# Kernel optimization log

Measured on AMD Instinct MI355X. Metric: run time of the kernel, lower is better.

The kernel has to match this reference:

```python
import jax, jax.numpy as jnp
import numpy as np

BLOCK = 128
FP8_MAX = 448.0  # max representable value of float8_e4m3fn
F8 = jnp.float8_e4m3fn


def setup_inputs() -> dict:
    key = jax.random.key(0)
    k1, k2, k3 = jax.random.split(key, 3)
    M, K, N = 4096, 7168, 16384
    x = jax.random.normal(k1, (M, K), jnp.float32)
    w = jax.random.normal(k2, (N, K), jnp.float32)  # raw weight; cast to fp8 in reference to simulate stored fp8
    w_scale = jax.random.uniform(k3, (N // BLOCK, K // BLOCK), jnp.float32, 0.5, 1.5)
    return {"x": x, "w": w, "w_scale": w_scale, "block_size": BLOCK}


def act_quant(x, b):
    M, K = x.shape
    xb = x.reshape(M, K // b, b)
    s = jnp.max(jnp.abs(xb), axis=-1) / FP8_MAX  # [M, K//b]
    xq = (xb / s[..., None]).astype(F8).astype(jnp.float32).reshape(M, K)
    return xq, s


def reference(x, w, w_scale, block_size):
    b = block_size
    # simulate fp8-stored weight (element_size == 1 branch)
    w8 = w.astype(F8).astype(jnp.float32)  # [N, K]
    # fp8_gemm: y[m,n] = sum_k xq[m,k]*w8[n,k]*xs[m,kb]*ws[nb,kb]
    # scales factor per-element, so dequantize both operands then one dense GEMM
    xq, xs = act_quant(x, b)
    x_dq = xq * jnp.repeat(xs, b, axis=1)                         # [M, K]
    w_dq = w8 * jnp.repeat(jnp.repeat(w_scale, b, axis=0), b, axis=1)  # [N, K]
    return x_dq @ w_dq.T  # [M, N], no bias (bias=False)
```

## Files before the change

kernel.cpp:

```cpp
#include <hip/hip_runtime.h>
#include <hip/hip_bf16.h>
#include <hip/hip_fp8.h>

typedef __attribute__((ext_vector_type(4))) float f32x4;
typedef __attribute__((ext_vector_type(2))) long long ll2;

#define AS1 __attribute__((address_space(1)))
#define AS3 __attribute__((address_space(3)))

static constexpr int Mdim = 4096;
static constexpr int Kdim = 7168;
static constexpr int Ndim = 16384;
static constexpr int KB   = Kdim / 128;
static constexpr float FP8_MAX = 448.0f;

#define BARRIER() do { asm volatile("" ::: "memory"); \
                       __builtin_amdgcn_s_barrier();  \
                       asm volatile("" ::: "memory"); } while (0)

#define MFMA_FP8 __builtin_amdgcn_mfma_f32_16x16x32_fp8_fp8

__global__ __launch_bounds__(256) void quant_x_kernel(
    const float* __restrict__ x, unsigned char* __restrict__ xq,
    float* __restrict__ xst)
{
    constexpr int NBLK = Mdim * KB;
    const int lane = threadIdx.x & 63;
    const int wid  = (blockIdx.x * 256 + threadIdx.x) >> 6;
    const int nw   = (gridDim.x * 256) >> 6;

    for (int b = wid; b < NBLK; b += nw) {
        size_t base = (size_t)b * 128 + lane * 2;
        float2 v = *reinterpret_cast<const float2*>(x + base);
        float amax = fmaxf(fabsf(v.x), fabsf(v.y));
#pragma unroll
        for (int off = 32; off > 0; off >>= 1)
            amax = fmaxf(amax, __shfl_xor(amax, off));
        float s = amax * (1.0f / FP8_MAX);
        unsigned char q0 = 0, q1 = 0;
        if (s > 0.0f) {
            q0 = __hip_fp8_e4m3(v.x / s).__x;
            q1 = __hip_fp8_e4m3(v.y / s).__x;
        }
        *reinterpret_cast<unsigned short*>(xq + base) =
            (unsigned short)(q0 | ((unsigned short)q1 << 8));
        if (lane == 0) {
            int row = b / KB, kb = b - row * KB;
            xst[(size_t)kb * Mdim + row] = s;
        }
    }
}

__global__ __launch_bounds__(256) void quant_w_kernel(
    const float* __restrict__ w, unsigned char* __restrict__ w8)
{
    constexpr size_t NCHUNK = (size_t)Ndim * Kdim / 8;

    size_t idx    = (size_t)blockIdx.x * 256 + threadIdx.x;
    size_t stride = (size_t)gridDim.x * 256;

    for (size_t c = idx; c < NCHUNK; c += stride) {
        const float* src = w + c * 8;
        float4 v0 = *reinterpret_cast<const float4*>(src);
        float4 v1 = *reinterpret_cast<const float4*>(src + 4);
        unsigned int lo = (unsigned int)__hip_fp8_e4m3(v0.x).__x
                        | ((unsigned int)__hip_fp8_e4m3(v0.y).__x << 8)
                        | ((unsigned int)__hip_fp8_e4m3(v0.z).__x << 16)
                        | ((unsigned int)__hip_fp8_e4m3(v0.w).__x << 24);
        unsigned int hi = (unsigned int)__hip_fp8_e4m3(v1.x).__x
                        | ((unsigned int)__hip_fp8_e4m3(v1.y).__x << 8)
                        | ((unsigned int)__hip_fp8_e4m3(v1.z).__x << 16)
                        | ((unsigned int)__hip_fp8_e4m3(v1.w).__x << 24);
        uint2 p; p.x = lo; p.y = hi;
        *reinterpret_cast<uint2*>(w8 + c * 8) = p;
    }
}

constexpr int BM = 256, BN = 256, BK = 64;
constexpr int NT  = Kdim / BK;
constexpr int NBN = Ndim / BN;
constexpr int NWG = (Mdim / BM) * NBN;
constexpr int K1  = Kdim;
constexpr int XS_OFF = 65536;
constexpr int WS_OFF = XS_OFF + 56 * 1024;
constexpr int LDS_TOT = WS_OFF + 448;

__global__ __launch_bounds__(512, 2) void gemm256_fp8_kernel(
    const unsigned char* __restrict__ Ag,
    const unsigned char* __restrict__ Bg,
    const float* __restrict__ xsT,
    const float* __restrict__ Wsc,
    float* __restrict__ C)
{
    extern __shared__ char smem[];

    const int tid  = threadIdx.x;
    const int w    = tid >> 6;
    const int lane = tid & 63;
    const int wr   = w >> 2;
    const int wc   = w & 3;
    const int lr   = lane & 15;
    const int lk   = lane >> 4;

    int bid = (int)blockIdx.x;
    int swz = (bid & 7) * (NWG >> 3) + (bid >> 3);
    const int bm = (swz / NBN) * BM;
    const int bn = (swz % NBN) * BN;

    const int colF = (lk ^ ((lr >> 1) & 3)) << 4;
    const int bRow = (wc & 1) * 64;

    const char* xsL0 = smem + XS_OFF + (wr * 128 + lk * 4) * 4;
    const char* wsL  = smem + WS_OFF + (wc >> 1) * (KB * 4);

    const int rowS = tid >> 2;
    const int colS = (((tid & 3) ^ ((rowS >> 1) & 3))) * 16;
    const size_t offG = (size_t)rowS * K1 + colS;
    const int ldsW = tid * 16;

    const char* Ab = (const char*)Ag + (size_t)bm * K1;
    const char* Bb = (const char*)Bg + (size_t)bn * K1;

    auto stage = [&](int j) {
        if (j >= 4 * NT) return;
        const int T    = j >> 2;
        const int r    = j & 3;
        const int isA  = r >> 1;
        const int half = r & 1;
        const int regByte = (T & 1) * 32768 + (isA ? 0 : 16384) + half * 8192;
        const char* g = (isA ? Ab : Bb) + (size_t)half * (128 * (size_t)K1)
                        + (size_t)T * 64 + offG;
        __builtin_amdgcn_global_load_lds((const AS1 void*)g,
                                         (AS3 void*)(smem + regByte + ldsW),
                                         16, 0, 0);
    };

#pragma unroll
    for (int i = 0; i < 7; ++i) {
        const int kb = w * 7 + i;
        const float* g = xsT + (size_t)kb * Mdim + bm + lane * 4;
        __builtin_amdgcn_global_load_lds((const AS1 void*)g,
            (AS3 void*)(smem + XS_OFF + kb * 1024), 16, 0, 0);
    }
    if (w == 0 && lane < 28) {
        const float* g = Wsc + (size_t)(bn >> 7) * KB + lane * 4;
        __builtin_amdgcn_global_load_lds((const AS1 void*)g,
            (AS3 void*)(smem + WS_OFF), 16, 0, 0);
    }
    for (int j = 0; j < 6; ++j) stage(j);
    asm volatile("s_waitcnt vmcnt(2)" ::: "memory");
    BARRIER();

    f32x4 acc[8][4] = {};

    for (int t = 0; t < NT; ++t) {
        const int buf = t & 1;
        const int kb  = t >> 1;
        const char* aB = smem + buf * 32768 + wr * 8192;
        const char* bB = smem + buf * 32768 + 16384 + (wc >> 1) * 8192;
        ll2 a0[4], a1[4], b0[2], b1[2];
        f32x4 sv[4];

        const float wsv  = *(const float*)(wsL + kb * 4);
        const char* xsLk = xsL0 + (kb << 10);

        stage(4 * t + 6);
#pragma unroll
        for (int m = 0; m < 4; ++m)
            a0[m] = *(const ll2*)(aB + (m * 16 + lr) * 64 + colF);
#pragma unroll
        for (int n = 0; n < 2; ++n)
            b0[n] = *(const ll2*)(bB + (bRow + n * 16 + lr) * 64 + colF);
#pragma unroll
        for (int m = 0; m < 4; ++m)
            sv[m] = *reinterpret_cast<const f32x4*>(xsLk + m * 64) * wsv;
        __builtin_amdgcn_s_setprio(1);
#pragma unroll
        for (int m = 0; m < 4; ++m)
#pragma unroll
            for (int n = 0; n < 2; ++n) {
                f32x4 pacc = {0.f, 0.f, 0.f, 0.f};
                pacc = MFMA_FP8(a0[m][0], b0[n][0], pacc, 0, 0, 0);
                pacc = MFMA_FP8(a0[m][1], b0[n][1], pacc, 0, 0, 0);
                acc[m][n] += sv[m] * pacc;
            }
        __builtin_amdgcn_s_setprio(0);

        stage(4 * t + 7);
#pragma unroll
        for (int n = 0; n < 2; ++n)
            b1[n] = *(const ll2*)(bB + (bRow + (n + 2) * 16 + lr) * 64 + colF);
        __builtin_amdgcn_s_setprio(1);
#pragma unroll
        for (int m = 0; m < 4; ++m)
#pragma unroll
            for (int n = 0; n < 2; ++n) {
                f32x4 pacc = {0.f, 0.f, 0.f, 0.f};
                pacc = MFMA_FP8(a0[m][0], b1[n][0], pacc, 0, 0, 0);
                pacc = MFMA_FP8(a0[m][1], b1[n][1], pacc, 0, 0, 0);
                acc[m][n + 2] += sv[m] * pacc;
            }
        __builtin_amdgcn_s_setprio(0);
        BARRIER();

        stage(4 * t + 8);
#pragma unroll
        for (int m = 0; m < 4; ++m)
            a1[m] = *(const ll2*)(aB + ((m + 4) * 16 + lr) * 64 + colF);
#pragma unroll
        for (int m = 0; m < 4; ++m)
            sv[m] = *reinterpret_cast<const f32x4*>(xsLk + 256 + m * 64) * wsv;
        __builtin_amdgcn_s_setprio(1);
#pragma unroll
        for (int m = 0; m < 4; ++m)
#pragma unroll
            for (int n = 0; n < 2; ++n) {
                f32x4 pacc = {0.f, 0.f, 0.f, 0.f};
                pacc = MFMA_FP8(a1[m][0], b0[n][0], pacc, 0, 0, 0);
                pacc = MFMA_FP8(a1[m][1], b0[n][1], pacc, 0, 0, 0);
                acc[m + 4][n] += sv[m] * pacc;
            }
        __builtin_amdgcn_s_setprio(0);

        stage(4 * t + 9);
        __builtin_amdgcn_s_setprio(1);
#pragma unroll
        for (int m = 0; m < 4; ++m)
#pragma unroll
            for (int n = 0; n < 2; ++n) {
                f32x4 pacc = {0.f, 0.f, 0.f, 0.f};
                pacc = MFMA_FP8(a1[m][0], b1[n][0], pacc, 0, 0, 0);
                pacc = MFMA_FP8(a1[m][1], b1[n][1], pacc, 0, 0, 0);
                acc[m + 4][n + 2] += sv[m] * pacc;
            }
        __builtin_amdgcn_s_setprio(0);
        if (t < NT - 2) { asm volatile("s_waitcnt vmcnt(2)" ::: "memory"); }
        else            { asm volatile("s_waitcnt vmcnt(0)" ::: "memory"); }
        BARRIER();
    }

#pragma unroll
    for (int m = 0; m < 8; ++m) {
#pragma unroll
        for (int n = 0; n < 4; ++n) {
            const int row0 = bm + wr * 128 + m * 16 + lk * 4;
            const int col  = bn + wc * 64 + n * 16 + lr;
#pragma unroll
            for (int j = 0; j < 4; ++j)
                C[(size_t)(row0 + j) * Ndim + col] = acc[m][n][j];
        }
    }
}

extern "C" void kernel_launch(void* const* d_in, const int* in_sizes, int n_in,
                              void* d_out, int out_size, void* d_ws, size_t ws_size,
                              hipStream_t stream) {
    const float* x  = (const float*)d_in[0];
    const float* w  = (const float*)d_in[1];
    const float* ws = (const float*)d_in[2];

    unsigned char* xq  = (unsigned char*)d_ws;
    unsigned char* w8  = xq + (size_t)Mdim * Kdim;
    float*         xst = (float*)(w8 + (size_t)Ndim * Kdim);

    quant_x_kernel<<<2048, 256, 0, stream>>>(x, xq, xst);
    quant_w_kernel<<<4096, 256, 0, stream>>>(w, w8);

    hipFuncSetAttribute((const void*)gemm256_fp8_kernel,
                        hipFuncAttributeMaxDynamicSharedMemorySize, LDS_TOT);
    gemm256_fp8_kernel<<<NWG, 512, LDS_TOT, stream>>>(xq, w8, xst, ws,
                                                      (float*)d_out);
}
```

Baseline: 1.044 ms.

## Shrink GEMM tile to 128x256 and restructure LDS staging pipeline

```diff
diff --git a/kernel.cpp b/kernel.cpp
--- a/kernel.cpp
+++ b/kernel.cpp
@@ -76,16 +76,17 @@
     }
 }
 
-constexpr int BM = 256, BN = 256, BK = 64;
+constexpr int BM = 128, BN = 256, BK = 64;
 constexpr int NT  = Kdim / BK;
 constexpr int NBN = Ndim / BN;
 constexpr int NWG = (Mdim / BM) * NBN;
 constexpr int K1  = Kdim;
-constexpr int XS_OFF = 65536;
-constexpr int WS_OFF = XS_OFF + 56 * 1024;
+constexpr int BUFSZ  = 24576;
+constexpr int XS_OFF = 49152;
+constexpr int WS_OFF = XS_OFF + 56 * 512;
 constexpr int LDS_TOT = WS_OFF + 448;
 
-__global__ __launch_bounds__(512, 2) void gemm256_fp8_kernel(
+__global__ __launch_bounds__(512, 2) void gemm128_fp8_kernel(
     const unsigned char* __restrict__ Ag,
     const unsigned char* __restrict__ Bg,
     const float* __restrict__ xsT,
@@ -108,27 +109,24 @@
     const int bn = (swz % NBN) * BN;
 
     const int colF = (lk ^ ((lr >> 1) & 3)) << 4;
+    const int aRow = wr * 64;
     const int bRow = (wc & 1) * 64;
 
-    const char* xsL0 = smem + XS_OFF + (wr * 128 + lk * 4) * 4;
+    const char* xsL0 = smem + XS_OFF + (wr * 64 + lk * 4) * 4;
     const char* wsL  = smem + WS_OFF + (wc >> 1) * (KB * 4);
 
     const int rowS = tid >> 2;
     const int colS = (((tid & 3) ^ ((rowS >> 1) & 3))) * 16;
     const size_t offG = (size_t)rowS * K1 + colS;
-    const int ldsW = tid * 16;
+    const int ldsW = w * 1024;
 
     const char* Ab = (const char*)Ag + (size_t)bm * K1;
     const char* Bb = (const char*)Bg + (size_t)bn * K1;
 
-    auto stage = [&](int j) {
-        if (j >= 4 * NT) return;
-        const int T    = j >> 2;
-        const int r    = j & 3;
-        const int isA  = r >> 1;
-        const int half = r & 1;
-        const int regByte = (T & 1) * 32768 + (isA ? 0 : 16384) + half * 8192;
-        const char* g = (isA ? Ab : Bb) + (size_t)half * (128 * (size_t)K1)
+    auto stage = [&](int T, int r) {
+        if (T >= NT) return;
+        const int regByte = (T & 1) * BUFSZ + r * 8192;
+        const char* g = (r ? Bb + (size_t)(r - 1) * (128 * (size_t)K1) : Ab)
                         + (size_t)T * 64 + offG;
         __builtin_amdgcn_global_load_lds((const AS1 void*)g,
                                          (AS3 void*)(smem + regByte + ldsW),
@@ -136,42 +134,50 @@
     };
 
 #pragma unroll
-    for (int i = 0; i < 7; ++i) {
-        const int kb = w * 7 + i;
-        const float* g = xsT + (size_t)kb * Mdim + bm + lane * 4;
-        __builtin_amdgcn_global_load_lds((const AS1 void*)g,
-            (AS3 void*)(smem + XS_OFF + kb * 1024), 16, 0, 0);
+    for (int i = 0; i < 4; ++i) {
+        const int c = i * 8 + w;
+        if (c < 28) {
+            const int kb  = 2 * c + (lane >> 5);
+            const int row = (lane & 31) * 4;
+            const float* g = xsT + (size_t)kb * Mdim + bm + row;
+            __builtin_amdgcn_global_load_lds((const AS1 void*)g,
+                (AS3 void*)(smem + XS_OFF + c * 1024), 16, 0, 0);
+        }
     }
     if (w == 0 && lane < 28) {
         const float* g = Wsc + (size_t)(bn >> 7) * KB + lane * 4;
         __builtin_amdgcn_global_load_lds((const AS1 void*)g,
             (AS3 void*)(smem + WS_OFF), 16, 0, 0);
     }
-    for (int j = 0; j < 6; ++j) stage(j);
+    stage(0, 0); stage(0, 1); stage(0, 2);
+    stage(1, 1); stage(1, 2);
     asm volatile("s_waitcnt vmcnt(2)" ::: "memory");
     BARRIER();
 
-    f32x4 acc[8][4] = {};
+    f32x4 acc[4][4] = {};
 
     for (int t = 0; t < NT; ++t) {
         const int buf = t & 1;
         const int kb  = t >> 1;
-        const char* aB = smem + buf * 32768 + wr * 8192;
-        const char* bB = smem + buf * 32768 + 16384 + (wc >> 1) * 8192;
-        ll2 a0[4], a1[4], b0[2], b1[2];
+        const char* aB = smem + buf * BUFSZ;
+        const char* bB = smem + buf * BUFSZ + 8192 + (wc >> 1) * 8192;
+        ll2 a[4], b0[2], b1[2];
         f32x4 sv[4];
 
         const float wsv  = *(const float*)(wsL + kb * 4);
-        const char* xsLk = xsL0 + (kb << 10);
-
-        stage(4 * t + 6);
-#pragma unroll
-        for (int m = 0; m < 4; ++m)
-            a0[m] = *(const ll2*)(aB + (m * 16 + lr) * 64 + colF);
+        const char* xsLk = xsL0 + kb * 512;
+
+        stage(t + 1, 0);
+#pragma unroll
+        for (int m = 0; m < 4; ++m)
+            a[m] = *(const ll2*)(aB + (aRow + m * 16 + lr) * 64 + colF);
 #pragma unroll
         for (int n = 0; n < 2; ++n)
             b0[n] = *(const ll2*)(bB + (bRow + n * 16 + lr) * 64 + colF);
 #pragma unroll
+        for (int n = 0; n < 2; ++n)
+            b1[n] = *(const ll2*)(bB + (bRow + (n + 2) * 16 + lr) * 64 + colF);
+#pragma unroll
         for (int m = 0; m < 4; ++m)
             sv[m] = *reinterpret_cast<const f32x4*>(xsLk + m * 64) * wsv;
         __builtin_amdgcn_s_setprio(1);
@@ -180,58 +186,25 @@
 #pragma unroll
             for (int n = 0; n < 2; ++n) {
                 f32x4 pacc = {0.f, 0.f, 0.f, 0.f};
-                pacc = MFMA_FP8(a0[m][0], b0[n][0], pacc, 0, 0, 0);
-                pacc = MFMA_FP8(a0[m][1], b0[n][1], pacc, 0, 0, 0);
+                pacc = MFMA_FP8(a[m][0], b0[n][0], pacc, 0, 0, 0);
+                pacc = MFMA_FP8(a[m][1], b0[n][1], pacc, 0, 0, 0);
                 acc[m][n] += sv[m] * pacc;
             }
         __builtin_amdgcn_s_setprio(0);
-
-        stage(4 * t + 7);
-#pragma unroll
-        for (int n = 0; n < 2; ++n)
-            b1[n] = *(const ll2*)(bB + (bRow + (n + 2) * 16 + lr) * 64 + colF);
+        asm volatile("s_waitcnt lgkmcnt(0)" ::: "memory");
+        BARRIER();
+
+        stage(t + 2, 1);
+        stage(t + 2, 2);
         __builtin_amdgcn_s_setprio(1);
 #pragma unroll
         for (int m = 0; m < 4; ++m)
 #pragma unroll
             for (int n = 0; n < 2; ++n) {
                 f32x4 pacc = {0.f, 0.f, 0.f, 0.f};
-                pacc = MFMA_FP8(a0[m][0], b1[n][0], pacc, 0, 0, 0);
-                pacc = MFMA_FP8(a0[m][1], b1[n][1], pacc, 0, 0, 0);
+                pacc = MFMA_FP8(a[m][0], b1[n][0], pacc, 0, 0, 0);
+                pacc = MFMA_FP8(a[m][1], b1[n][1], pacc, 0, 0, 0);
                 acc[m][n + 2] += sv[m] * pacc;
-            }
-        __builtin_amdgcn_s_setprio(0);
-        BARRIER();
-
-        stage(4 * t + 8);
-#pragma unroll
-        for (int m = 0; m < 4; ++m)
-            a1[m] = *(const ll2*)(aB + ((m + 4) * 16 + lr) * 64 + colF);
-#pragma unroll
-        for (int m = 0; m < 4; ++m)
-            sv[m] = *reinterpret_cast<const f32x4*>(xsLk + 256 + m * 64) * wsv;
-        __builtin_amdgcn_s_setprio(1);
-#pragma unroll
-        for (int m = 0; m < 4; ++m)
-#pragma unroll
-            for (int n = 0; n < 2; ++n) {
-                f32x4 pacc = {0.f, 0.f, 0.f, 0.f};
-                pacc = MFMA_FP8(a1[m][0], b0[n][0], pacc, 0, 0, 0);
-                pacc = MFMA_FP8(a1[m][1], b0[n][1], pacc, 0, 0, 0);
-                acc[m + 4][n] += sv[m] * pacc;
-            }
-        __builtin_amdgcn_s_setprio(0);
-
-        stage(4 * t + 9);
-        __builtin_amdgcn_s_setprio(1);
-#pragma unroll
-        for (int m = 0; m < 4; ++m)
-#pragma unroll
-            for (int n = 0; n < 2; ++n) {
-                f32x4 pacc = {0.f, 0.f, 0.f, 0.f};
-                pacc = MFMA_FP8(a1[m][0], b1[n][0], pacc, 0, 0, 0);
-                pacc = MFMA_FP8(a1[m][1], b1[n][1], pacc, 0, 0, 0);
-                acc[m + 4][n + 2] += sv[m] * pacc;
             }
         __builtin_amdgcn_s_setprio(0);
         if (t < NT - 2) { asm volatile("s_waitcnt vmcnt(2)" ::: "memory"); }
@@ -240,10 +213,10 @@
     }
 
 #pragma unroll
-    for (int m = 0; m < 8; ++m) {
+    for (int m = 0; m < 4; ++m) {
 #pragma unroll
         for (int n = 0; n < 4; ++n) {
-            const int row0 = bm + wr * 128 + m * 16 + lk * 4;
+            const int row0 = bm + wr * 64 + m * 16 + lk * 4;
             const int col  = bn + wc * 64 + n * 16 + lr;
 #pragma unroll
             for (int j = 0; j < 4; ++j)
@@ -266,8 +239,8 @@
     quant_x_kernel<<<2048, 256, 0, stream>>>(x, xq, xst);
     quant_w_kernel<<<4096, 256, 0, stream>>>(w, w8);
 
-    hipFuncSetAttribute((const void*)gemm256_fp8_kernel,
+    hipFuncSetAttribute((const void*)gemm128_fp8_kernel,
                         hipFuncAttributeMaxDynamicSharedMemorySize, LDS_TOT);
-    gemm256_fp8_kernel<<<NWG, 512, LDS_TOT, stream>>>(xq, w8, xst, ws,
+    gemm128_fp8_kernel<<<NWG, 512, LDS_TOT, stream>>>(xq, w8, xst, ws,
                                                       (float*)d_out);
 }
```

Measured after the change: 1.067 ms. 2.2% more time.
